# Performance work log

Hardware: AMD Instinct MI355X
Metric: run time of the kernel (lower is better)

The kernel has to match this reference:

```python
import jax, jax.numpy as jnp
import numpy as np

ALPHA = 0.2        # LeakyReLU negative slope
NEG = -9e15        # mask value used by the torch module
N, FIN, H, D = 4096, 20, 4, 64


def gat_layer(h, adj_mask, W, a_src, a_dst, average):
    """Multi-head GAT layer. W: [H,Fin,Fout], a_src/a_dst: [H,Fout].
    e_ij = LeakyReLU(a_src . Wh_i + a_dst . Wh_j) == a^T [Wh_i || Wh_j],
    identical math to the N x N x 2F concat in the torch code, without
    materializing the pairwise concat tensor."""
    Wh = jnp.einsum('nf,hfo->hno', h, W)                 # [H,N,F]
    f_s = jnp.einsum('hno,ho->hn', Wh, a_src)            # [H,N]
    f_d = jnp.einsum('hno,ho->hn', Wh, a_dst)            # [H,N]
    e = jax.nn.leaky_relu(f_s[:, :, None] + f_d[:, None, :], ALPHA)  # [H,N,N]
    e = jnp.where(adj_mask[None], e, NEG)
    att = jax.nn.softmax(e, axis=-1)
    out = jax.nn.elu(jnp.einsum('hnm,hmo->hno', att, Wh))  # per-head ELU (concat=True inside)
    if average:
        return out.mean(axis=0)                           # [N,F]
    return jnp.transpose(out, (1, 0, 2)).reshape(h.shape[0], -1)  # [N,H*F]


def setup_inputs() -> dict:
    key = jax.random.key(0)
    ks = jax.random.split(key, 6)
    x = jax.random.normal(ks[0], (N, FIN), jnp.float32)
    adj = jax.random.randint(ks[1], (N, N), 0, 2, jnp.int32)
    # layer 0: 20 -> 64 per head, 4 heads, concat -> 256
    W0 = jax.random.normal(ks[2], (H, FIN, D), jnp.float32) * 0.3
    a0 = jax.random.normal(ks[3], (H, 2 * D), jnp.float32) * 0.1
    # layer 1: 256 -> 64 per head, heads averaged
    W1 = jax.random.normal(ks[4], (H, H * D, D), jnp.float32) * 0.06
    a1 = jax.random.normal(ks[5], (H, 2 * D), jnp.float32) * 0.1
    return {"x": x, "adj": adj, "W0": W0, "a0": a0, "W1": W1, "a1": a1}


def reference(x, adj, W0, a0, W1, a1):
    mask = adj > 0
    h = gat_layer(x, mask, W0, a0[:, :D], a0[:, D:], average=False)   # [N, 256]
    return gat_layer(h, mask, W1, a1[:, :D], a1[:, D:], average=True)  # [N, 64]
```

## Files before the change

### kernel.cpp

```cpp
#include <hip/hip_runtime.h>
#include <hip/hip_fp16.h>
#include <math.h>

#define NN 4096
#define FIN 20
#define NH 4
#define DH 64
#define ALPHA 0.2f
#define LOG2E 1.4426950408889634f

typedef _Float16 f16x8 __attribute__((ext_vector_type(8)));
typedef _Float16 f16x4 __attribute__((ext_vector_type(4)));
typedef float f32x4 __attribute__((ext_vector_type(4)));

__device__ inline void gload_lds16(const void* gsrc, void* ldsbase) {
    __builtin_amdgcn_global_load_lds(
        (const __attribute__((address_space(1))) void*)gsrc,
        (__attribute__((address_space(3))) void*)ldsbase, 16, 0, 0);
}

__global__ __launch_bounds__(256) void k_pack(const int* __restrict__ adj,
        unsigned char* __restrict__ bits) {
    int t = blockIdx.x * 256 + threadIdx.x;
    const int4* p = (const int4*)(adj + (size_t)t * 8);
    int4 a = p[0], b = p[1];
    unsigned int byte = 0;
    byte |= (a.x > 0) << 0; byte |= (a.y > 0) << 1;
    byte |= (a.z > 0) << 2; byte |= (a.w > 0) << 3;
    byte |= (b.x > 0) << 4; byte |= (b.y > 0) << 5;
    byte |= (b.z > 0) << 6; byte |= (b.w > 0) << 7;
    bits[t] = (unsigned char)byte;
}

__global__ __launch_bounds__(256) void k_l0wh(const float* __restrict__ x,
        const float* __restrict__ W0, const float* __restrict__ a0,
        _Float16* __restrict__ whT, float* __restrict__ fs, float* __restrict__ fd) {
    __shared__ float xs[16 * FIN];
    int n0 = blockIdx.x * 16;
    int tid = threadIdx.x;
    for (int i = tid; i < 16 * FIN; i += 256) xs[i] = x[n0 * FIN + i];
    __syncthreads();
    int h = tid >> 6, d = tid & 63;
    float w0r[FIN];
#pragma unroll
    for (int f = 0; f < FIN; ++f) w0r[f] = W0[(h * FIN + f) * DH + d];
    float asrc = a0[h * 2 * DH + d];
    float adst = a0[h * 2 * DH + DH + d];
    f16x8 wv[2];
#pragma unroll
    for (int n = 0; n < 16; ++n) {
        float wh = 0.f;
#pragma unroll
        for (int f = 0; f < FIN; ++f) wh = fmaf(xs[n * FIN + f], w0r[f], wh);
        wv[n >> 3][n & 7] = (_Float16)wh;
        float sv = wh * asrc, dv = wh * adst;
#pragma unroll
        for (int off = 1; off <= 32; off <<= 1) {
            sv += __shfl_xor(sv, off);
            dv += __shfl_xor(dv, off);
        }
        if (d == 0) { fs[h * NN + n0 + n] = sv; fd[h * NN + n0 + n] = dv; }
    }
    _Float16* dst = whT + ((size_t)(h * DH + d) * NN + n0);
    *(f16x8*)(dst) = wv[0];
    *(f16x8*)(dst + 8) = wv[1];
}

__global__ __launch_bounds__(256) void k_fdmax(const float* __restrict__ fd,
        float* __restrict__ fdm) {
    int h = blockIdx.x, tid = threadIdx.x;
    float m = -3e38f;
    for (int i = tid; i < NN; i += 256) m = fmaxf(m, fd[h * NN + i]);
#pragma unroll
    for (int off = 1; off <= 32; off <<= 1) m = fmaxf(m, __shfl_xor(m, off));
    __shared__ float mx[4];
    if ((tid & 63) == 0) mx[tid >> 6] = m;
    __syncthreads();
    if (tid == 0) fdm[h] = fmaxf(fmaxf(mx[0], mx[1]), fmaxf(mx[2], mx[3]));
}

__global__ void k_w1t(const float* __restrict__ W1, _Float16* __restrict__ w1T) {
    int u = blockIdx.x * 256 + threadIdx.x;
    int h = u >> 14, f = (u >> 6) & 255, d = u & 63;
    w1T[((size_t)(h * DH + d) << 8) + f] = (_Float16)W1[u];
}

__global__ __launch_bounds__(512) void k_attn(const float* __restrict__ fs,
        const float* __restrict__ fd, const float* __restrict__ fdmax,
        const _Float16* __restrict__ whT, const unsigned char* __restrict__ bits,
        float* __restrict__ pv, float* __restrict__ pl) {
    __shared__ __align__(16) char smem[33280];
    const int ch = blockIdx.x & 1;
    const int rowblk = (blockIdx.x >> 1) & 63;
    const int h = blockIdx.x >> 7;
    const int row0 = rowblk << 6;
    const int cb0 = ch << 11;
    const int tid = threadIdx.x;
    const int l = tid & 63, w = tid >> 6;
    const int rl = l & 15, g = l >> 4;
    const int rg = w >> 2, cq = w & 3;
    const int r0 = row0 + rg * 32 + rl;
    const int r1 = r0 + 16;
    const float fsr0 = fs[h * NN + r0], fsr1 = fs[h * NN + r1];
    const float fm = fdmax[h];
    const float su0 = fsr0 + fm, su1 = fsr1 + fm;
    const float m0 = fmaxf(su0, ALPHA * su0);
    const float m1 = fmaxf(su1, ALPHA * su1);
    const float A0 = (fsr0 - m0) * LOG2E, B0 = (ALPHA * fsr0 - m0) * LOG2E;
    const float A1 = (fsr1 - m1) * LOG2E, B1 = (ALPHA * fsr1 - m1) * LOG2E;
    const float* fdp = fd + h * NN + cb0 + cq * 32 + g * 8;
    const unsigned char* bp0 = bits + (size_t)r0 * (NN / 8) + (cb0 >> 3) + cq * 4;
    const unsigned char* bp1 = bits + (size_t)r1 * (NN / 8) + (cb0 >> 3) + cq * 4;
    const _Float16* whb = whT + (size_t)h * DH * NN + cb0;

    const int tpp0 = tid, tpp1 = 512 + tid;
    const int d0_ = tpp0 >> 4, c0_ = tpp0 & 15;
    const int d1_ = tpp1 >> 4, c1_ = tpp1 & 15;
    const _Float16* src0 = whb + (size_t)d0_ * NN + 8 * (c0_ ^ (d0_ & 7));
    const _Float16* src1 = whb + (size_t)d1_ * NN + 8 * (c1_ ^ (d1_ & 7));
    char* dstA0 = smem + w * 1024;
    char* dstA1 = smem + 8192 + w * 1024;
    char* dstB0 = smem + 16384 + w * 1024;
    char* dstB1 = smem + 16384 + 8192 + w * 1024;

    f32x4 acc0[4] = {{0,0,0,0},{0,0,0,0},{0,0,0,0},{0,0,0,0}};
    f32x4 acc1[4] = {{0,0,0,0},{0,0,0,0},{0,0,0,0},{0,0,0,0}};
    f32x4 al0 = {0,0,0,0}, al1 = {0,0,0,0};
    f16x8 ones;
#pragma unroll
    for (int i = 0; i < 8; ++i) ones[i] = (_Float16)1.0f;
    const int rdswz = (cq * 64 + g * 16) ^ ((rl & 7) << 4);

    gload_lds16(src0, dstA0);
    gload_lds16(src1, dstA1);
    float4 faA = *(const float4*)(fdp);
    float4 fbA = *(const float4*)(fdp + 4);
    unsigned int mA0 = *(const unsigned int*)(bp0);
    unsigned int mA1 = *(const unsigned int*)(bp1);
    float4 faB, fbB;
    unsigned int mB0, mB1;
    __syncthreads();

#define COMPUTE(BUF, FA, FB, M0v, M1v)                                          \
    {                                                                           \
        const float fv[8] = {FA.x, FA.y, FA.z, FA.w, FB.x, FB.y, FB.z, FB.w};   \
        f16x8 av0, av1;                                                         \
        const int sh = g << 3;                                                  \
        _Pragma("unroll")                                                       \
        for (int i = 0; i < 8; ++i) {                                           \
            float t0 = fmaxf(fmaf(fv[i], LOG2E, A0), fmaf(fv[i], ALPHA * LOG2E, B0)); \
            t0 = ((M0v >> (sh + i)) & 1u) ? t0 : -1e30f;                        \
            av0[i] = (_Float16)exp2f(t0);                                       \
            float t1 = fmaxf(fmaf(fv[i], LOG2E, A1), fmaf(fv[i], ALPHA * LOG2E, B1)); \
            t1 = ((M1v >> (sh + i)) & 1u) ? t1 : -1e30f;                        \
            av1[i] = (_Float16)exp2f(t1);                                       \
        }                                                                       \
        al0 = __builtin_amdgcn_mfma_f32_16x16x32_f16(av0, ones, al0, 0, 0, 0);  \
        al1 = __builtin_amdgcn_mfma_f32_16x16x32_f16(av1, ones, al1, 0, 0, 0);  \
        _Pragma("unroll")                                                       \
        for (int t4 = 0; t4 < 4; ++t4) {                                        \
            f16x8 bv = *(const f16x8*)(BUF + ((16 * t4 + rl) << 8) + rdswz);    \
            acc0[t4] = __builtin_amdgcn_mfma_f32_16x16x32_f16(av0, bv, acc0[t4], 0, 0, 0); \
            acc1[t4] = __builtin_amdgcn_mfma_f32_16x16x32_f16(av1, bv, acc1[t4], 0, 0, 0); \
        }                                                                       \
    }

#pragma unroll 1
    for (int k = 0; k < 8; ++k) {
        const int tB = 2 * k + 1;
        gload_lds16(src0 + tB * 128, dstB0);
        gload_lds16(src1 + tB * 128, dstB1);
        faB = *(const float4*)(fdp + tB * 128);
        fbB = *(const float4*)(fdp + tB * 128 + 4);
        mB0 = *(const unsigned int*)(bp0 + tB * 16);
        mB1 = *(const unsigned int*)(bp1 + tB * 16);
        COMPUTE(smem, faA, fbA, mA0, mA1);
        __syncthreads();
        if (k < 7) {
            const int tA = 2 * k + 2;
            gload_lds16(src0 + tA * 128, dstA0);
            gload_lds16(src1 + tA * 128, dstA1);
            faA = *(const float4*)(fdp + tA * 128);
            fbA = *(const float4*)(fdp + tA * 128 + 4);
            mA0 = *(const unsigned int*)(bp0 + tA * 16);
            mA1 = *(const unsigned int*)(bp1 + tA * 16);
        }
        COMPUTE((smem + 16384), faB, fbB, mB0, mB1);
        __syncthreads();
    }
#undef COMPUTE

    float* red = (float*)smem;
    float* lred = (float*)(smem + 32768);
#pragma unroll
    for (int p = 0; p < 2; ++p) {
        if (rg == p) {
#pragma unroll
            for (int t4 = 0; t4 < 4; ++t4)
#pragma unroll
                for (int i = 0; i < 4; ++i) {
                    red[(cq * 32 + 4 * g + i) * 64 + 16 * t4 + rl]      = acc0[t4][i];
                    red[(cq * 32 + 16 + 4 * g + i) * 64 + 16 * t4 + rl] = acc1[t4][i];
                }
            if (rl == 0) {
#pragma unroll
                for (int i = 0; i < 4; ++i) {
                    lred[cq * 32 + 4 * g + i]      = al0[i];
                    lred[cq * 32 + 16 + 4 * g + i] = al1[i];
                }
            }
        }
        __syncthreads();
#pragma unroll
        for (int j = 0; j < 4; ++j) {
            const int R = w * 4 + j;
            float v = 0.f, L = 0.f;
#pragma unroll
            for (int cc = 0; cc < 4; ++cc) {
                v += red[(cc * 32 + R) * 64 + l];
                L += lred[cc * 32 + R];
            }
            const int Rg = row0 + p * 32 + R;
            pv[(((size_t)(ch * NH + h) * NN) + Rg) * 64 + l] = v;
            if (l == 0) pl[(size_t)(ch * NH + h) * NN + Rg] = L;
        }
        __syncthreads();
    }
}

template<int MODE>
__global__ __launch_bounds__(256) void k_merge(const float* __restrict__ pv,
        const float* __restrict__ pl, void* __restrict__ outp) {
    int t = blockIdx.x * 256 + threadIdx.x;
    if (MODE == 0) {
        int d = t & 63, n = (t >> 6) & (NN - 1), h = t >> 18;
        float v = pv[((size_t)h * NN + n) * 64 + d] + pv[((size_t)(NH + h) * NN + n) * 64 + d];
        float L = pl[h * NN + n] + pl[NH * NN + h * NN + n];
        float o = v * __builtin_amdgcn_rcpf(L);
        o = o > 0.f ? o : __expf(o) - 1.f;
        ((_Float16*)outp)[(size_t)n * (NH * DH) + h * DH + d] = (_Float16)o;
    } else {
        int d = t & 63, n = t >> 6;
        float s = 0.f;
#pragma unroll
        for (int h = 0; h < NH; ++h) {
            float v = pv[((size_t)h * NN + n) * 64 + d] + pv[((size_t)(NH + h) * NN + n) * 64 + d];
            float L = pl[h * NN + n] + pl[NH * NN + h * NN + n];
            float o = v * __builtin_amdgcn_rcpf(L);
            s += o > 0.f ? o : __expf(o) - 1.f;
        }
        ((float*)outp)[t] = 0.25f * s;
    }
}

__global__ __launch_bounds__(256) void k_l1wh(const _Float16* __restrict__ h16,
        const _Float16* __restrict__ w1T, const float* __restrict__ a1,
        _Float16* __restrict__ whT, float* __restrict__ fs, float* __restrict__ fd) {
    __shared__ float red[4][16][64];
    __shared__ _Float16 lt[16][64];
    int h = blockIdx.x >> 8;
    int row0 = (blockIdx.x & 255) << 4;
    int tid = threadIdx.x;
    int l = tid & 63, w = tid >> 6;
    int rl = l & 15, g = l >> 4;
    f32x4 acc[4] = {{0,0,0,0},{0,0,0,0},{0,0,0,0},{0,0,0,0}};
    const _Float16* ap = h16 + (size_t)(row0 + rl) * (NH * DH) + w * 64;
    const _Float16* bp = w1T + ((size_t)h * DH << 8) + w * 64;
#pragma unroll
    for (int j = 0; j < 2; ++j) {
        int fb = j * 32 + 8 * g;
        f16x8 avv = *(const f16x8*)(ap + fb);
#pragma unroll
        for (int t4 = 0; t4 < 4; ++t4) {
            f16x8 bv = *(const f16x8*)(bp + ((size_t)(16 * t4 + rl) << 8) + fb);
            acc[t4] = __builtin_amdgcn_mfma_f32_16x16x32_f16(avv, bv, acc[t4], 0, 0, 0);
        }
    }
#pragma unroll
    for (int t4 = 0; t4 < 4; ++t4)
#pragma unroll
        for (int i = 0; i < 4; ++i) red[w][t4 * 4 + i][l] = acc[t4][i];
    __syncthreads();
#pragma unroll
    for (int i = 0; i < 4; ++i) {
        float v = red[0][w * 4 + i][l] + red[1][w * 4 + i][l]
                + red[2][w * 4 + i][l] + red[3][w * 4 + i][l];
        lt[4 * g + i][16 * w + rl] = (_Float16)v;
    }
    __syncthreads();
    int d = tid & 63, rb = tid >> 6;
    f16x4 o;
#pragma unroll
    for (int j = 0; j < 4; ++j) o[j] = lt[rb * 4 + j][d];
    *(f16x4*)(whT + (size_t)(h * DH + d) * NN + row0 + rb * 4) = o;
    float as_ = a1[h * 2 * DH + d], ad_ = a1[h * 2 * DH + DH + d];
    float svj[4], dvj[4];
#pragma unroll
    for (int j = 0; j < 4; ++j) {
        float wv = (float)lt[rb * 4 + j][d];
        svj[j] = wv * as_;
        dvj[j] = wv * ad_;
    }
#pragma unroll
    for (int off = 1; off <= 32; off <<= 1) {
#pragma unroll
        for (int j = 0; j < 4; ++j) {
            svj[j] += __shfl_xor(svj[j], off);
            dvj[j] += __shfl_xor(dvj[j], off);
        }
    }
    if (d == 0) {
#pragma unroll
        for (int j = 0; j < 4; ++j) {
            fs[h * NN + row0 + rb * 4 + j] = svj[j];
            fd[h * NN + row0 + rb * 4 + j] = dvj[j];
        }
    }
}

extern "C" void kernel_launch(void* const* d_in, const int* in_sizes, int n_in,
                              void* d_out, int out_size, void* d_ws, size_t ws_size,
                              hipStream_t stream) {
    const float* x  = (const float*)d_in[0];
    const int* adj  = (const int*)d_in[1];
    const float* W0 = (const float*)d_in[2];
    const float* a0 = (const float*)d_in[3];
    const float* W1 = (const float*)d_in[4];
    const float* a1 = (const float*)d_in[5];
    float* out = (float*)d_out;
    char* ws = (char*)d_ws;

    unsigned char* bits = (unsigned char*)(ws);
    _Float16* whT0 = (_Float16*)(ws + (2ull << 20));
    _Float16* h16  = (_Float16*)(ws + (4ull << 20));
    _Float16* w1T  = (_Float16*)(ws + (6ull << 20));
    _Float16* whT1 = (_Float16*)(ws + (6ull << 20) + (256ull << 10));
    float* fs0  = (float*)(ws + (9ull << 20));
    float* fd0  = fs0 + NH * NN;
    float* fs1  = fd0 + NH * NN;
    float* fd1  = fs1 + NH * NN;
    float* fdm0 = fd1 + NH * NN;
    float* fdm1 = fdm0 + 8;
    float* pv   = (float*)(ws + (10ull << 20));
    float* pl   = (float*)(ws + (18ull << 20));

    k_pack<<<NN * NN / 8 / 256, 256, 0, stream>>>(adj, bits);
    k_w1t<<<(NH * NH * DH * DH) / 256, 256, 0, stream>>>(W1, w1T);
    k_l0wh<<<NN / 16, 256, 0, stream>>>(x, W0, a0, whT0, fs0, fd0);
    k_fdmax<<<NH, 256, 0, stream>>>(fd0, fdm0);
    k_attn<<<2 * NH * (NN / 64), 512, 0, stream>>>(fs0, fd0, fdm0, whT0, bits, pv, pl);
    k_merge<0><<<(NH * NN * DH) / 256, 256, 0, stream>>>(pv, pl, h16);
    k_l1wh<<<NH * (NN / 16), 256, 0, stream>>>(h16, w1T, a1, whT1, fs1, fd1);
    k_fdmax<<<NH, 256, 0, stream>>>(fd1, fdm1);
    k_attn<<<2 * NH * (NN / 64), 512, 0, stream>>>(fs1, fd1, fdm1, whT1, bits, pv, pl);
    k_merge<1><<<(NN * DH) / 256, 256, 0, stream>>>(pv, pl, out);
}
```

Measured before the change: 124.0 us.

## Merge front kernels, deepen attention prefetch pipeline, pack fp16 converts, pad reduction LDS

Three small setup kernels (adjacency bit-pack, layer-0 projection, W1 transpose) become one launch that branches on block index. The attention loop now keeps two tiles in flight, using explicit vmcnt waits and raw barriers in place of full __syncthreads. The exp results are converted with packed round-toward-zero fp16 conversion, and the reduction scratch gets a row stride of 66 to avoid LDS bank conflicts. Together these target launch overhead, memory latency stalls and LDS conflicts. The cost is fragile hand-counted waitcnt logic and slightly different fp16 rounding.

```diff
diff --git a/kernel.cpp b/kernel.cpp
--- a/kernel.cpp
+++ b/kernel.cpp
@@ -11,6 +11,7 @@
 
 typedef _Float16 f16x8 __attribute__((ext_vector_type(8)));
 typedef _Float16 f16x4 __attribute__((ext_vector_type(4)));
+typedef __fp16 fp16x2 __attribute__((ext_vector_type(2)));
 typedef float f32x4 __attribute__((ext_vector_type(4)));
 
 __device__ inline void gload_lds16(const void* gsrc, void* ldsbase) {
@@ -19,51 +20,57 @@
         (__attribute__((address_space(3))) void*)ldsbase, 16, 0, 0);
 }
 
-__global__ __launch_bounds__(256) void k_pack(const int* __restrict__ adj,
-        unsigned char* __restrict__ bits) {
-    int t = blockIdx.x * 256 + threadIdx.x;
-    const int4* p = (const int4*)(adj + (size_t)t * 8);
-    int4 a = p[0], b = p[1];
-    unsigned int byte = 0;
-    byte |= (a.x > 0) << 0; byte |= (a.y > 0) << 1;
-    byte |= (a.z > 0) << 2; byte |= (a.w > 0) << 3;
-    byte |= (b.x > 0) << 4; byte |= (b.y > 0) << 5;
-    byte |= (b.z > 0) << 6; byte |= (b.w > 0) << 7;
-    bits[t] = (unsigned char)byte;
-}
-
-__global__ __launch_bounds__(256) void k_l0wh(const float* __restrict__ x,
+__global__ __launch_bounds__(256) void k_front(const int* __restrict__ adj,
+        unsigned char* __restrict__ bits, const float* __restrict__ x,
         const float* __restrict__ W0, const float* __restrict__ a0,
-        _Float16* __restrict__ whT, float* __restrict__ fs, float* __restrict__ fd) {
+        _Float16* __restrict__ whT, float* __restrict__ fs, float* __restrict__ fd,
+        const float* __restrict__ W1, _Float16* __restrict__ w1T) {
     __shared__ float xs[16 * FIN];
-    int n0 = blockIdx.x * 16;
-    int tid = threadIdx.x;
-    for (int i = tid; i < 16 * FIN; i += 256) xs[i] = x[n0 * FIN + i];
-    __syncthreads();
-    int h = tid >> 6, d = tid & 63;
-    float w0r[FIN];
-#pragma unroll
-    for (int f = 0; f < FIN; ++f) w0r[f] = W0[(h * FIN + f) * DH + d];
-    float asrc = a0[h * 2 * DH + d];
-    float adst = a0[h * 2 * DH + DH + d];
-    f16x8 wv[2];
-#pragma unroll
-    for (int n = 0; n < 16; ++n) {
-        float wh = 0.f;
-#pragma unroll
-        for (int f = 0; f < FIN; ++f) wh = fmaf(xs[n * FIN + f], w0r[f], wh);
-        wv[n >> 3][n & 7] = (_Float16)wh;
-        float sv = wh * asrc, dv = wh * adst;
-#pragma unroll
-        for (int off = 1; off <= 32; off <<= 1) {
-            sv += __shfl_xor(sv, off);
-            dv += __shfl_xor(dv, off);
-        }
-        if (d == 0) { fs[h * NN + n0 + n] = sv; fd[h * NN + n0 + n] = dv; }
-    }
-    _Float16* dst = whT + ((size_t)(h * DH + d) * NN + n0);
-    *(f16x8*)(dst) = wv[0];
-    *(f16x8*)(dst + 8) = wv[1];
+    const int bid = blockIdx.x;
+    const int tid = threadIdx.x;
+    if (bid < 8192) {
+        int t = bid * 256 + tid;
+        const int4* p = (const int4*)(adj + (size_t)t * 8);
+        int4 a = p[0], b = p[1];
+        unsigned int byte = 0;
+        byte |= (a.x > 0) << 0; byte |= (a.y > 0) << 1;
+        byte |= (a.z > 0) << 2; byte |= (a.w > 0) << 3;
+        byte |= (b.x > 0) << 4; byte |= (b.y > 0) << 5;
+        byte |= (b.z > 0) << 6; byte |= (b.w > 0) << 7;
+        bits[t] = (unsigned char)byte;
+    } else if (bid < 8448) {
+        int n0 = (bid - 8192) * 16;
+        for (int i = tid; i < 16 * FIN; i += 256) xs[i] = x[n0 * FIN + i];
+        __syncthreads();
+        int h = tid >> 6, d = tid & 63;
+        float w0r[FIN];
+#pragma unroll
+        for (int f = 0; f < FIN; ++f) w0r[f] = W0[(h * FIN + f) * DH + d];
+        float asrc = a0[h * 2 * DH + d];
+        float adst = a0[h * 2 * DH + DH + d];
+        f16x8 wv[2];
+#pragma unroll
+        for (int n = 0; n < 16; ++n) {
+            float wh = 0.f;
+#pragma unroll
+            for (int f = 0; f < FIN; ++f) wh = fmaf(xs[n * FIN + f], w0r[f], wh);
+            wv[n >> 3][n & 7] = (_Float16)wh;
+            float sv = wh * asrc, dv = wh * adst;
+#pragma unroll
+            for (int off = 1; off <= 32; off <<= 1) {
+                sv += __shfl_xor(sv, off);
+                dv += __shfl_xor(dv, off);
+            }
+            if (d == 0) { fs[h * NN + n0 + n] = sv; fd[h * NN + n0 + n] = dv; }
+        }
+        _Float16* dst = whT + ((size_t)(h * DH + d) * NN + n0);
+        *(f16x8*)(dst) = wv[0];
+        *(f16x8*)(dst + 8) = wv[1];
+    } else {
+        int u = (bid - 8448) * 256 + tid;
+        int h = u >> 14, f = (u >> 6) & 255, d = u & 63;
+        w1T[((size_t)(h * DH + d) << 8) + f] = (_Float16)W1[u];
+    }
 }
 
 __global__ __launch_bounds__(256) void k_fdmax(const float* __restrict__ fd,
@@ -79,17 +86,11 @@
     if (tid == 0) fdm[h] = fmaxf(fmaxf(mx[0], mx[1]), fmaxf(mx[2], mx[3]));
 }
 
-__global__ void k_w1t(const float* __restrict__ W1, _Float16* __restrict__ w1T) {
-    int u = blockIdx.x * 256 + threadIdx.x;
-    int h = u >> 14, f = (u >> 6) & 255, d = u & 63;
-    w1T[((size_t)(h * DH + d) << 8) + f] = (_Float16)W1[u];
-}
-
 __global__ __launch_bounds__(512) void k_attn(const float* __restrict__ fs,
         const float* __restrict__ fd, const float* __restrict__ fdmax,
         const _Float16* __restrict__ whT, const unsigned char* __restrict__ bits,
         float* __restrict__ pv, float* __restrict__ pl) {
-    __shared__ __align__(16) char smem[33280];
+    __shared__ __align__(16) char smem[34304];
     const int ch = blockIdx.x & 1;
     const int rowblk = (blockIdx.x >> 1) & 63;
     const int h = blockIdx.x >> 7;
@@ -113,15 +114,10 @@
     const unsigned char* bp1 = bits + (size_t)r1 * (NN / 8) + (cb0 >> 3) + cq * 4;
     const _Float16* whb = whT + (size_t)h * DH * NN + cb0;
 
-    const int tpp0 = tid, tpp1 = 512 + tid;
-    const int d0_ = tpp0 >> 4, c0_ = tpp0 & 15;
-    const int d1_ = tpp1 >> 4, c1_ = tpp1 & 15;
+    const int d0_ = tid >> 4, c0_ = tid & 15;
+    const int d1_ = (512 + tid) >> 4, c1_ = tid & 15;
     const _Float16* src0 = whb + (size_t)d0_ * NN + 8 * (c0_ ^ (d0_ & 7));
     const _Float16* src1 = whb + (size_t)d1_ * NN + 8 * (c1_ ^ (d1_ & 7));
-    char* dstA0 = smem + w * 1024;
-    char* dstA1 = smem + 8192 + w * 1024;
-    char* dstB0 = smem + 16384 + w * 1024;
-    char* dstB1 = smem + 16384 + 8192 + w * 1024;
 
     f32x4 acc0[4] = {{0,0,0,0},{0,0,0,0},{0,0,0,0},{0,0,0,0}};
     f32x4 acc1[4] = {{0,0,0,0},{0,0,0,0},{0,0,0,0},{0,0,0,0}};
@@ -131,67 +127,82 @@
     for (int i = 0; i < 8; ++i) ones[i] = (_Float16)1.0f;
     const int rdswz = (cq * 64 + g * 16) ^ ((rl & 7) << 4);
 
-    gload_lds16(src0, dstA0);
-    gload_lds16(src1, dstA1);
-    float4 faA = *(const float4*)(fdp);
-    float4 fbA = *(const float4*)(fdp + 4);
-    unsigned int mA0 = *(const unsigned int*)(bp0);
-    unsigned int mA1 = *(const unsigned int*)(bp1);
-    float4 faB, fbB;
-    unsigned int mB0, mB1;
-    __syncthreads();
-
-#define COMPUTE(BUF, FA, FB, M0v, M1v)                                          \
+    float4 faA, fbA, faB, fbB;
+    unsigned int mA0, mA1, mB0, mB1;
+
+#define STAGE(BOFF, T)                                                          \
+    gload_lds16(src0 + (T) * 128, smem + (BOFF) + w * 1024);                    \
+    gload_lds16(src1 + (T) * 128, smem + (BOFF) + 8192 + w * 1024);
+
+#define FEED(FA, FB, M0v, M1v, T)                                               \
+    FA = *(const float4*)(fdp + (T) * 128);                                     \
+    FB = *(const float4*)(fdp + (T) * 128 + 4);                                 \
+    M0v = *(const unsigned int*)(bp0 + (T) * 16);                               \
+    M1v = *(const unsigned int*)(bp1 + (T) * 16);
+
+#define COMPUTE(BOFF, FA, FB, M0v, M1v)                                         \
     {                                                                           \
+        const char* buf_ = smem + (BOFF);                                       \
         const float fv[8] = {FA.x, FA.y, FA.z, FA.w, FB.x, FB.y, FB.z, FB.w};   \
         f16x8 av0, av1;                                                         \
         const int sh = g << 3;                                                  \
         _Pragma("unroll")                                                       \
-        for (int i = 0; i < 8; ++i) {                                           \
-            float t0 = fmaxf(fmaf(fv[i], LOG2E, A0), fmaf(fv[i], ALPHA * LOG2E, B0)); \
-            t0 = ((M0v >> (sh + i)) & 1u) ? t0 : -1e30f;                        \
-            av0[i] = (_Float16)exp2f(t0);                                       \
-            float t1 = fmaxf(fmaf(fv[i], LOG2E, A1), fmaf(fv[i], ALPHA * LOG2E, B1)); \
-            t1 = ((M1v >> (sh + i)) & 1u) ? t1 : -1e30f;                        \
-            av1[i] = (_Float16)exp2f(t1);                                       \
+        for (int i = 0; i < 8; i += 2) {                                        \
+            float ta = fmaxf(fmaf(fv[i], LOG2E, A0), fmaf(fv[i], ALPHA * LOG2E, B0)); \
+            ta = ((M0v >> (sh + i)) & 1u) ? ta : -1e30f;                        \
+            float tb = fmaxf(fmaf(fv[i+1], LOG2E, A0), fmaf(fv[i+1], ALPHA * LOG2E, B0)); \
+            tb = ((M0v >> (sh + i + 1)) & 1u) ? tb : -1e30f;                    \
+            fp16x2 p0 = __builtin_amdgcn_cvt_pkrtz(exp2f(ta), exp2f(tb));       \
+            av0[i] = (_Float16)p0[0]; av0[i+1] = (_Float16)p0[1];               \
+            float tc = fmaxf(fmaf(fv[i], LOG2E, A1), fmaf(fv[i], ALPHA * LOG2E, B1)); \
+            tc = ((M1v >> (sh + i)) & 1u) ? tc : -1e30f;                        \
+            float td = fmaxf(fmaf(fv[i+1], LOG2E, A1), fmaf(fv[i+1], ALPHA * LOG2E, B1)); \
+            td = ((M1v >> (sh + i + 1)) & 1u) ? td : -1e30f;                    \
+            fp16x2 p1 = __builtin_amdgcn_cvt_pkrtz(exp2f(tc), exp2f(td));       \
+            av1[i] = (_Float16)p1[0]; av1[i+1] = (_Float16)p1[1];               \
         }                                                                       \
         al0 = __builtin_amdgcn_mfma_f32_16x16x32_f16(av0, ones, al0, 0, 0, 0);  \
         al1 = __builtin_amdgcn_mfma_f32_16x16x32_f16(av1, ones, al1, 0, 0, 0);  \
         _Pragma("unroll")                                                       \
         for (int t4 = 0; t4 < 4; ++t4) {                                        \
-            f16x8 bv = *(const f16x8*)(BUF + ((16 * t4 + rl) << 8) + rdswz);    \
+            f16x8 bv = *(const f16x8*)(buf_ + ((16 * t4 + rl) << 8) + rdswz);   \
             acc0[t4] = __builtin_amdgcn_mfma_f32_16x16x32_f16(av0, bv, acc0[t4], 0, 0, 0); \
             acc1[t4] = __builtin_amdgcn_mfma_f32_16x16x32_f16(av1, bv, acc1[t4], 0, 0, 0); \
         }                                                                       \
     }
 
+#define WAIT6 asm volatile("s_waitcnt vmcnt(6)" ::: "memory");                  \
+    __builtin_amdgcn_s_barrier();                                               \
+    __builtin_amdgcn_sched_barrier(0);
+
+    STAGE(0, 0);      FEED(faA, fbA, mA0, mA1, 0);
+    STAGE(16384, 1);  FEED(faB, fbB, mB0, mB1, 1);
+
 #pragma unroll 1
-    for (int k = 0; k < 8; ++k) {
-        const int tB = 2 * k + 1;
-        gload_lds16(src0 + tB * 128, dstB0);
-        gload_lds16(src1 + tB * 128, dstB1);
-        faB = *(const float4*)(fdp + tB * 128);
-        fbB = *(const float4*)(fdp + tB * 128 + 4);
-        mB0 = *(const unsigned int*)(bp0 + tB * 16);
-        mB1 = *(const unsigned int*)(bp1 + tB * 16);
-        COMPUTE(smem, faA, fbA, mA0, mA1);
-        __syncthreads();
-        if (k < 7) {
-            const int tA = 2 * k + 2;
-            gload_lds16(src0 + tA * 128, dstA0);
-            gload_lds16(src1 + tA * 128, dstA1);
-            faA = *(const float4*)(fdp + tA * 128);
-            fbA = *(const float4*)(fdp + tA * 128 + 4);
-            mA0 = *(const unsigned int*)(bp0 + tA * 16);
-            mA1 = *(const unsigned int*)(bp1 + tA * 16);
-        }
-        COMPUTE((smem + 16384), faB, fbB, mB0, mB1);
-        __syncthreads();
-    }
+    for (int k = 0; k < 7; ++k) {
+        WAIT6
+        COMPUTE(0, faA, fbA, mA0, mA1);
+        __builtin_amdgcn_s_barrier();
+        STAGE(0, 2 * k + 2);  FEED(faA, fbA, mA0, mA1, 2 * k + 2);
+        WAIT6
+        COMPUTE(16384, faB, fbB, mB0, mB1);
+        __builtin_amdgcn_s_barrier();
+        STAGE(16384, 2 * k + 3);  FEED(faB, fbB, mB0, mB1, 2 * k + 3);
+    }
+    WAIT6
+    COMPUTE(0, faA, fbA, mA0, mA1);
+    asm volatile("s_waitcnt vmcnt(0)" ::: "memory");
+    __builtin_amdgcn_s_barrier();
+    __builtin_amdgcn_sched_barrier(0);
+    COMPUTE(16384, faB, fbB, mB0, mB1);
+    __syncthreads();
+#undef WAIT6
 #undef COMPUTE
+#undef FEED
+#undef STAGE
 
     float* red = (float*)smem;
-    float* lred = (float*)(smem + 32768);
+    float* lred = (float*)(smem + 33792);
 #pragma unroll
     for (int p = 0; p < 2; ++p) {
         if (rg == p) {
@@ -199,8 +210,8 @@
             for (int t4 = 0; t4 < 4; ++t4)
 #pragma unroll
                 for (int i = 0; i < 4; ++i) {
-                    red[(cq * 32 + 4 * g + i) * 64 + 16 * t4 + rl]      = acc0[t4][i];
-                    red[(cq * 32 + 16 + 4 * g + i) * 64 + 16 * t4 + rl] = acc1[t4][i];
+                    red[(cq * 32 + 4 * g + i) * 66 + 16 * t4 + rl]      = acc0[t4][i];
+                    red[(cq * 32 + 16 + 4 * g + i) * 66 + 16 * t4 + rl] = acc1[t4][i];
                 }
             if (rl == 0) {
 #pragma unroll
@@ -217,7 +228,7 @@
             float v = 0.f, L = 0.f;
 #pragma unroll
             for (int cc = 0; cc < 4; ++cc) {
-                v += red[(cc * 32 + R) * 64 + l];
+                v += red[(cc * 32 + R) * 66 + l];
                 L += lred[cc * 32 + R];
             }
             const int Rg = row0 + p * 32 + R;
@@ -344,9 +355,7 @@
     float* pv   = (float*)(ws + (10ull << 20));
     float* pl   = (float*)(ws + (18ull << 20));
 
-    k_pack<<<NN * NN / 8 / 256, 256, 0, stream>>>(adj, bits);
-    k_w1t<<<(NH * NH * DH * DH) / 256, 256, 0, stream>>>(W1, w1T);
-    k_l0wh<<<NN / 16, 256, 0, stream>>>(x, W0, a0, whT0, fs0, fd0);
+    k_front<<<8704, 256, 0, stream>>>(adj, bits, x, W0, a0, whT0, fs0, fd0, W1, w1T);
     k_fdmax<<<NH, 256, 0, stream>>>(fd0, fdm0);
     k_attn<<<2 * NH * (NN / 64), 512, 0, stream>>>(fs0, fd0, fdm0, whT0, bits, pv, pl);
     k_merge<0><<<(NH * NN * DH) / 256, 256, 0, stream>>>(pv, pl, h16);
```

Measured after the change: 134.0 us. 8.1% more time.
